# Optimization experiments

Measured on AMD Instinct MI355X. Metric: run time of the kernel, lower is better.

The kernel has to match this reference:

```python
import jax, jax.numpy as jnp
import numpy as np

HEADS = 8


def setup_inputs() -> dict:
    key = jax.random.key(0)
    ks = jax.random.split(key, 4)
    b, n, dim, inner = 8, 1024, 512, 512
    x = jax.random.normal(ks[0], (b, n, dim), jnp.float32)
    cp_mask = jax.random.randint(ks[1], (n, n), 0, 2, jnp.int32)  # binary core-periphery mask
    w_qkv = jax.random.normal(ks[2], (dim, 3 * inner), jnp.float32) * 0.02
    w_out = jax.random.normal(ks[3], (inner, dim), jnp.float32) * 0.02
    b_out = jnp.zeros((dim,), jnp.float32)
    return {"x": x, "cp_mask": cp_mask, "w_qkv": w_qkv, "w_out": w_out,
            "b_out": b_out, "patches_in_core_nodes": 16}


def reference(x, cp_mask, w_qkv, w_out, b_out, patches_in_core_nodes):
    b, n, dim = x.shape
    inner = w_qkv.shape[1] // 3
    dh = inner // HEADS
    scale = dh ** -0.5

    qkv = x @ w_qkv                                   # [b, n, 3*inner]
    q, k, v = jnp.split(qkv, 3, axis=-1)
    split_heads = lambda t: t.reshape(b, n, HEADS, dh).transpose(0, 2, 1, 3)
    q, k, v = map(split_heads, (q, k, v))             # [b, h, n, dh]

    mask = cp_mask.astype(x.dtype)                    # [n, n]
    dots_raw = jnp.einsum('bhnd,bhmd->bhnm', q, k)    # [b, h, n, n]

    # analysis pass: per-row mean |masked score|, summed over heads (detached in original)
    nnz = jnp.count_nonzero(cp_mask, axis=1).astype(x.dtype)       # [n]
    score = (jnp.abs(dots_raw * mask) * scale).sum(axis=1).sum(axis=-1) / nnz  # [b, n]
    score = jax.lax.stop_gradient(score)
    # original: list(np.argsort(score)) then list.reverse() -> batch order reversed
    idx = jnp.argsort(score, axis=-1)[::-1]           # [b, n]

    attn = jax.nn.softmax(dots_raw * scale * mask, axis=-1)
    out = jnp.einsum('bhnm,bhmd->bhnd', attn, v)      # [b, h, n, dh]
    out = out.transpose(0, 2, 1, 3).reshape(b, n, inner)

    # sequential row swap: out[j,i] <-> out[j,idx[j,i]] using the pristine clone
    out_clone = out
    bi = jnp.arange(b)
    for i in range(1, patches_in_core_nodes + 1):
        ti = idx[:, i]                                # [b]
        out = out.at[bi, i].set(out_clone[bi, ti])
        out = out.at[bi, ti].set(out_clone[:, i])
    return out @ w_out + b_out
```

## Files before the change

### kernel.cpp

```cpp
#include <hip/hip_runtime.h>
#include <hip/hip_bf16.h>

#define NN 1024
#define DH 64
#define DIM 512
#define INNER 512
#define QKV_N 1536
#define SCALE 0.125f
#define PPITCH 72

typedef short short8 __attribute__((ext_vector_type(8)));
typedef float floatx4 __attribute__((ext_vector_type(4)));

static __device__ __forceinline__ unsigned short f2bf(float x) {
  __hip_bfloat16 h = __float2bfloat16(x);
  unsigned short u;
  __builtin_memcpy(&u, &h, 2);
  return u;
}
static __device__ __forceinline__ void splitbf(float x, unsigned short& hi, unsigned short& lo) {
  __hip_bfloat16 h = __float2bfloat16(x);
  float hf = __bfloat162float(h);
  __hip_bfloat16 l = __float2bfloat16(x - hf);
  __builtin_memcpy(&hi, &h, 2);
  __builtin_memcpy(&lo, &l, 2);
}
static __device__ __forceinline__ void gll16(const unsigned short* g, unsigned short* l) {
  __builtin_amdgcn_global_load_lds(
      (const __attribute__((address_space(1))) unsigned int*)g,
      (__attribute__((address_space(3))) unsigned int*)l, 16, 0, 0);
}

__global__ __launch_bounds__(64) void nnz_kernel(const int* __restrict__ mask,
                                                 float* __restrict__ nnzf,
                                                 unsigned long long* __restrict__ Mbits) {
  int row = blockIdx.x;
  int lane = threadIdx.x;
  const int* mrow = mask + (size_t)row * NN;
  int tot = 0;
  for (int mt = 0; mt < 16; ++mt) {
    unsigned long long bits = __ballot(mrow[mt * 64 + lane] != 0);
    if (lane == 0) {
      Mbits[(size_t)mt * NN + row] = bits;
      tot += __popcll(bits);
    }
  }
  if (lane == 0) nnzf[row] = (float)tot;
}

__global__ __launch_bounds__(256) void split_kernel(const float* __restrict__ in,
                                                    unsigned short* __restrict__ hi,
                                                    unsigned short* __restrict__ lo,
                                                    int n4) {
  int i = blockIdx.x * 256 + threadIdx.x;
  if (i >= n4) return;
  float4 v = ((const float4*)in)[i];
  ushort4 h, l;
  splitbf(v.x, h.x, l.x);
  splitbf(v.y, h.y, l.y);
  splitbf(v.z, h.z, l.z);
  splitbf(v.w, h.w, l.w);
  ((ushort4*)hi)[i] = h;
  ((ushort4*)lo)[i] = l;
}

__global__ __launch_bounds__(256) void tsplit_kernel(const float* __restrict__ in, int K, int N,
                                                     unsigned short* __restrict__ hiT,
                                                     unsigned short* __restrict__ loT) {
  __shared__ float tile[32][33];
  int n0 = blockIdx.x * 32, k0 = blockIdx.y * 32;
  int t = threadIdx.x;
  int tn = t & 31, tk = t >> 5;
#pragma unroll
  for (int i = 0; i < 32; i += 8)
    tile[tk + i][tn] = in[(size_t)(k0 + tk + i) * N + n0 + tn];
  __syncthreads();
#pragma unroll
  for (int i = 0; i < 32; i += 8) {
    int n = tk + i;
    float v = tile[tn][n];
    unsigned short h, l;
    splitbf(v, h, l);
    hiT[(size_t)(n0 + n) * K + k0 + tn] = h;
    loT[(size_t)(n0 + n) * K + k0 + tn] = l;
  }
}

__global__ __launch_bounds__(256) void qkv_mfma(const unsigned short* __restrict__ xhi,
                                                const unsigned short* __restrict__ xlo,
                                                const unsigned short* __restrict__ bhiT,
                                                const unsigned short* __restrict__ bloT,
                                                unsigned short* __restrict__ qhi,
                                                unsigned short* __restrict__ qlo,
                                                unsigned short* __restrict__ khi,
                                                unsigned short* __restrict__ klo,
                                                unsigned short* __restrict__ vT) {
  __shared__ __align__(16) unsigned char smemQ[67584];
  unsigned short* planeS = (unsigned short*)smemQ;
  float* ct = (float*)smemQ;

  int l = blockIdx.x;
  int by = l & 63, bx = l >> 6;
  int r0 = by * 128, c0 = bx * 128;
  int which = c0 >> 9;
  bool split3 = (which != 2);
  int t = threadIdx.x;
  int lane = t & 63, w = t >> 6;
  int wr = w >> 1, wc = w & 1;
  int s = lane & 15, q4 = lane >> 4;
  int sx7 = s & 7;
  int r8 = lane >> 3, j7 = lane & 7;
  int colsw = ((j7 ^ r8) << 3);

  const unsigned short* gsrc;
  int tb;
  if (w == 0) { gsrc = xhi; tb = r0; }
  else if (w == 1) { gsrc = xlo; tb = r0; }
  else if (w == 2) { gsrc = bhiT; tb = c0; }
  else { gsrc = bloT; tb = c0; }
  unsigned short* lp = planeS + w * 8192;
  const unsigned short* gp = gsrc + (size_t)(tb + r8) * DIM + colsw;
  bool doStage = split3 || (w == 0) || (w == 2);

  const unsigned short* Ah = planeS;
  const unsigned short* Al = planeS + 8192;
  const unsigned short* Bh = planeS + 16384;
  const unsigned short* Bl = planeS + 24576;

  floatx4 acc[4][4];
#pragma unroll
  for (int mi = 0; mi < 4; ++mi)
#pragma unroll
    for (int ni = 0; ni < 4; ++ni) { acc[mi][ni][0] = 0.f; acc[mi][ni][1] = 0.f; acc[mi][ni][2] = 0.f; acc[mi][ni][3] = 0.f; }

  for (int kt = 0; kt < DIM; kt += 64) {
    __syncthreads();
    if (doStage) {
#pragma unroll
      for (int ii = 0; ii < 16; ++ii)
        gll16(gp + (size_t)ii * 8 * DIM + kt, lp + ii * 512);
    }
    __syncthreads();
#pragma unroll
    for (int ks2 = 0; ks2 < 2; ++ks2) {
      int pc = ((ks2 * 4 + q4) ^ sx7) << 3;
      short8 ah[4], al[4], bhf[4], blf[4];
#pragma unroll
      for (int mi = 0; mi < 4; ++mi) {
        int ra = (wr * 64 + mi * 16 + s) * 64 + pc;
        ah[mi] = *(const short8*)&Ah[ra];
        if (split3) al[mi] = *(const short8*)&Al[ra];
      }
#pragma unroll
      for (int ni = 0; ni < 4; ++ni) {
        int rb = (wc * 64 + ni * 16 + s) * 64 + pc;
        bhf[ni] = *(const short8*)&Bh[rb];
        if (split3) blf[ni] = *(const short8*)&Bl[rb];
      }
#pragma unroll
      for (int mi = 0; mi < 4; ++mi)
#pragma unroll
        for (int ni = 0; ni < 4; ++ni) {
          if (split3) {
            acc[mi][ni] = __builtin_amdgcn_mfma_f32_16x16x32_bf16(al[mi], bhf[ni], acc[mi][ni], 0, 0, 0);
            acc[mi][ni] = __builtin_amdgcn_mfma_f32_16x16x32_bf16(ah[mi], blf[ni], acc[mi][ni], 0, 0, 0);
          }
          acc[mi][ni] = __builtin_amdgcn_mfma_f32_16x16x32_bf16(ah[mi], bhf[ni], acc[mi][ni], 0, 0, 0);
        }
    }
  }

  __syncthreads();
  if (which != 2) {
    float sc = (which == 0) ? SCALE : 1.0f;
#pragma unroll
    for (int mi = 0; mi < 4; ++mi)
#pragma unroll
      for (int ni = 0; ni < 4; ++ni)
#pragma unroll
        for (int i = 0; i < 4; ++i)
          ct[(wr * 64 + mi * 16 + q4 * 4 + i) * 132 + (wc * 64 + ni * 16 + s)] = acc[mi][ni][i] * sc;
  } else {
#pragma unroll
    for (int mi = 0; mi < 4; ++mi)
#pragma unroll
      for (int ni = 0; ni < 4; ++ni)
#pragma unroll
        for (int i = 0; i < 4; ++i)
          ct[(wc * 64 + ni * 16 + s) * 132 + (wr * 64 + mi * 16 + q4 * 4 + i)] = acc[mi][ni][i];
  }
  __syncthreads();
  if (which != 2) {
    int tr = t >> 1, ch = t & 1;
    int R = r0 + tr, b = R >> 10, n = R & 1023;
    int h0 = ((c0 & 511) >> 6) + ch;
    unsigned short* dhi = (which == 0) ? qhi : khi;
    unsigned short* dlo = (which == 0) ? qlo : klo;
    size_t go = ((size_t)(((b << 3) + h0) << 10) + n) * DH;
#pragma unroll
    for (int u = 0; u < 4; ++u) {
      const float* src = &ct[tr * 132 + ch * 64 + u * 16];
      short8 h8a, h8b, l8a, l8b;
#pragma unroll
      for (int e = 0; e < 8; ++e) {
        unsigned short hh, ll;
        splitbf(src[e], hh, ll);
        h8a[e] = (short)hh; l8a[e] = (short)ll;
        splitbf(src[8 + e], hh, ll);
        h8b[e] = (short)hh; l8b[e] = (short)ll;
      }
      *(short8*)&dhi[go + u * 16] = h8a;
      *(short8*)&dhi[go + u * 16 + 8] = h8b;
      *(short8*)&dlo[go + u * 16] = l8a;
      *(short8*)&dlo[go + u * 16 + 8] = l8b;
    }
  } else {
    int cr = t >> 1, th = t & 1;
    int b = r0 >> 10;
    int hglob = ((c0 & 511) >> 6) + (cr >> 6);
    int d = cr & 63;
    int n0 = (r0 & 1023) + th * 64;
    size_t go = ((size_t)(((b << 3) + hglob) * DH) + d) * NN + n0;
#pragma unroll
    for (int u = 0; u < 4; ++u) {
      const float* src = &ct[cr * 132 + th * 64 + u * 16];
      short8 o0, o1;
#pragma unroll
      for (int e = 0; e < 8; ++e) {
        o0[e] = (short)f2bf(src[e]);
        o1[e] = (short)f2bf(src[8 + e]);
      }
      *(short8*)&vT[go + u * 16] = o0;
      *(short8*)&vT[go + u * 16 + 8] = o1;
    }
  }
}

__global__ __launch_bounds__(256, 4) void attn_kernel(const unsigned short* __restrict__ qhi,
                                                      const unsigned short* __restrict__ qlo,
                                                      const unsigned short* __restrict__ khi,
                                                      const unsigned short* __restrict__ klo,
                                                      const unsigned short* __restrict__ vT,
                                                      const unsigned long long* __restrict__ MbT,
                                                      unsigned short* __restrict__ ohi,
                                                      unsigned short* __restrict__ olo,
                                                      float* __restrict__ sph) {
  int l = blockIdx.y * 16 + blockIdx.x;
  int k = l >> 3;
  int rb = k & 15;
  int bh = (l & 7) + 8 * (k >> 4);
  int b = bh >> 3, h = bh & 7;
  int row0 = rb * 64;
  int t = threadIdx.x;
  int lane = t & 63, w = t >> 6;
  int q4 = lane >> 4, s = lane & 15;
  int sx7 = s & 7;
  int gr = 16 * w + s;
  int r8 = lane >> 3, j7 = lane & 7;
  int colsw = ((j7 ^ r8) << 3);

  __shared__ __align__(16) unsigned short stageS[3 * 4096];
  __shared__ __align__(16) unsigned short Ps[64 * PPITCH];
  __shared__ unsigned long long Mb[64];
  unsigned short* Khs = stageS;
  unsigned short* Kls = stageS + 4096;
  unsigned short* Vts = stageS + 8192;
  float* Ofl = (float*)stageS;

  const unsigned short* khp = khi + ((size_t)bh * NN + 16 * w + r8) * DH + colsw;
  const unsigned short* klp = klo + ((size_t)bh * NN + 16 * w + r8) * DH + colsw;
  const unsigned short* vtp = vT + ((size_t)bh * DH + 16 * w + r8) * NN + colsw;

  short8 aqh[2], aql[2];
  {
    size_t qb0 = ((size_t)bh * NN + row0 + gr) * DH;
#pragma unroll
    for (int ks = 0; ks < 2; ++ks) {
      aqh[ks] = *(const short8*)&qhi[qb0 + ks * 32 + q4 * 8];
      aql[ks] = *(const short8*)&qlo[qb0 + ks * 32 + q4 * 8];
    }
  }

  floatx4 Oacc[4];
  float Lacc[4], Sco[4];
#pragma unroll
  for (int j = 0; j < 4; ++j) { Oacc[j][0] = 0.f; Oacc[j][1] = 0.f; Oacc[j][2] = 0.f; Oacc[j][3] = 0.f; }
#pragma unroll
  for (int i = 0; i < 4; ++i) { Lacc[i] = 0.f; Sco[i] = 0.f; }

  for (int mt = 0; mt < 16; ++mt) {
    __syncthreads();
#pragma unroll
    for (int ii = 0; ii < 2; ++ii) {
      int lofs = (16 * w + 8 * ii) * 64;
      gll16(khp + (size_t)mt * 64 * DH + (size_t)ii * 8 * DH, Khs + lofs);
      gll16(klp + (size_t)mt * 64 * DH + (size_t)ii * 8 * DH, Kls + lofs);
      gll16(vtp + (size_t)mt * 64 + (size_t)ii * 8 * NN, Vts + lofs);
    }
    if (t < 64) Mb[t] = MbT[(size_t)mt * NN + row0 + t];
    __syncthreads();

    floatx4 Sf[4];
#pragma unroll
    for (int j = 0; j < 4; ++j) { Sf[j][0] = 0.f; Sf[j][1] = 0.f; Sf[j][2] = 0.f; Sf[j][3] = 0.f; }
#pragma unroll
    for (int ks = 0; ks < 2; ++ks) {
      int pc = ((ks * 4 + q4) ^ sx7) << 3;
#pragma unroll
      for (int j = 0; j < 4; ++j) {
        int rk = (16 * j + s) * 64 + pc;
        short8 kh8 = *(const short8*)&Khs[rk];
        short8 kl8 = *(const short8*)&Kls[rk];
        Sf[j] = __builtin_amdgcn_mfma_f32_16x16x32_bf16(aql[ks], kh8, Sf[j], 0, 0, 0);
        Sf[j] = __builtin_amdgcn_mfma_f32_16x16x32_bf16(aqh[ks], kl8, Sf[j], 0, 0, 0);
        Sf[j] = __builtin_amdgcn_mfma_f32_16x16x32_bf16(aqh[ks], kh8, Sf[j], 0, 0, 0);
      }
    }

    unsigned long long mb[4];
#pragma unroll
    for (int i = 0; i < 4; ++i) mb[i] = Mb[16 * w + 4 * q4 + i];
    unsigned short pw[4][4];
#pragma unroll
    for (int j = 0; j < 4; ++j) {
#pragma unroll
      for (int i = 0; i < 4; ++i) {
        float sv = Sf[j][i];
        float mf = ((mb[i] >> (16 * j + s)) & 1ULL) ? 1.0f : 0.0f;
        Sco[i] += fabsf(sv) * mf;
        float p = __expf(sv * mf);
        Lacc[i] += p;
        pw[i][j] = f2bf(p);
      }
    }

#pragma unroll
    for (int i = 0; i < 4; ++i)
#pragma unroll
      for (int j = 0; j < 4; ++j) Ps[(16 * w + 4 * q4 + i) * PPITCH + 16 * j + s] = pw[i][j];

#pragma unroll
    for (int ks = 0; ks < 2; ++ks) {
      int mm0 = ks * 32 + q4 * 8;
      short8 ap = *(const short8*)&Ps[gr * PPITCH + mm0];
      int pc = ((ks * 4 + q4) ^ sx7) << 3;
#pragma unroll
      for (int j = 0; j < 4; ++j) {
        short8 bv = *(const short8*)&Vts[(16 * j + s) * 64 + pc];
        Oacc[j] = __builtin_amdgcn_mfma_f32_16x16x32_bf16(ap, bv, Oacc[j], 0, 0, 0);
      }
    }
  }

#pragma unroll
  for (int off = 1; off < 16; off <<= 1) {
#pragma unroll
    for (int i = 0; i < 4; ++i) {
      Lacc[i] += __shfl_xor(Lacc[i], off, 16);
      Sco[i] += __shfl_xor(Sco[i], off, 16);
    }
  }
  if (s == 0) {
#pragma unroll
    for (int i = 0; i < 4; ++i)
      sph[((size_t)bh << 10) + row0 + 16 * w + 4 * q4 + i] = Sco[i];
  }

  __syncthreads();
#pragma unroll
  for (int i = 0; i < 4; ++i) {
    float iv = 1.0f / Lacc[i];
#pragma unroll
    for (int j = 0; j < 4; ++j)
      Ofl[(16 * w + 4 * q4 + i) * 68 + 16 * j + s] = Oacc[j][i] * iv;
  }
  __syncthreads();
  {
    int tr = t >> 2, dq = t & 3;
    int r = row0 + tr;
    size_t go = ((size_t)((b << 10) + r)) * INNER + (h << 6) + dq * 16;
    const float* src = &Ofl[tr * 68 + dq * 16];
    short8 h8a, h8b, l8a, l8b;
#pragma unroll
    for (int e = 0; e < 8; ++e) {
      unsigned short hh, ll;
      splitbf(src[e], hh, ll);
      h8a[e] = (short)hh; l8a[e] = (short)ll;
      splitbf(src[8 + e], hh, ll);
      h8b[e] = (short)hh; l8b[e] = (short)ll;
    }
    *(short8*)&ohi[go] = h8a;
    *(short8*)&ohi[go + 8] = h8b;
    *(short8*)&olo[go] = l8a;
    *(short8*)&olo[go + 8] = l8b;
  }
}

__global__ __launch_bounds__(256) void score_select(const float* __restrict__ sph,
                                                    const float* __restrict__ nnzf,
                                                    const int* __restrict__ pic_ptr,
                                                    int* __restrict__ asc) {
  int bb = blockIdx.x;
  int t = threadIdx.x;
  int cnt = pic_ptr[0] + 1;
  float v[4];
#pragma unroll
  for (int i = 0; i < 4; ++i) {
    int r = t + 256 * i;
    float sv = 0.f;
#pragma unroll
    for (int h = 0; h < 8; ++h) sv += sph[(size_t)(((bb << 3) + h) << 10) + r];
    v[i] = sv / nnzf[r];
  }
  __shared__ float wv[4];
  __shared__ int wi[4];
  __shared__ int bsel;
  for (int sel = 0; sel < cnt; ++sel) {
    float bv = v[0];
    int bi = t;
#pragma unroll
    for (int i = 1; i < 4; ++i) {
      if (v[i] < bv) { bv = v[i]; bi = t + 256 * i; }
    }
#pragma unroll
    for (int off = 1; off < 64; off <<= 1) {
      float ov = __shfl_xor(bv, off, 64);
      int oi = __shfl_xor(bi, off, 64);
      if (ov < bv || (ov == bv && oi < bi)) { bv = ov; bi = oi; }
    }
    if ((t & 63) == 0) { wv[t >> 6] = bv; wi[t >> 6] = bi; }
    __syncthreads();
    if (t == 0) {
      float B = wv[0]; int I = wi[0];
#pragma unroll
      for (int q = 1; q < 4; ++q) {
        if (wv[q] < B || (wv[q] == B && wi[q] < I)) { B = wv[q]; I = wi[q]; }
      }
      bsel = I;
      asc[bb * 32 + sel] = I;
    }
    __syncthreads();
    int wloc = bsel - t;
    if (wloc >= 0 && (wloc & 255) == 0 && wloc < 1024) v[wloc >> 8] = 3.4e38f;
    __syncthreads();
  }
}

__global__ __launch_bounds__(256) void build_src(const int* __restrict__ asc,
                                                 const int* __restrict__ pic_ptr,
                                                 int* __restrict__ src) {
  int bi = blockIdx.x;
  int t = threadIdx.x;
  for (int r = t; r < 1024; r += 256) src[bi * 1024 + r] = r;
  __syncthreads();
  if (t == 0) {
    int pic = pic_ptr[0];
    const int* a = &asc[(7 - bi) * 32];
    for (int i = 1; i <= pic; ++i) {
      int ti = a[i];
      src[bi * 1024 + i] = ti;
      src[bi * 1024 + ti] = i;
    }
  }
}

__global__ __launch_bounds__(256) void out_mfma(const unsigned short* __restrict__ ahi,
                                                const unsigned short* __restrict__ alo,
                                                const unsigned short* __restrict__ bhiT,
                                                const unsigned short* __restrict__ bloT,
                                                const float* __restrict__ bias,
                                                const int* __restrict__ src,
                                                float* __restrict__ C) {
  __shared__ __align__(16) unsigned short planeS[4 * 8192];
  int l = blockIdx.x;
  int by = l & 63, bx = l >> 6;
  int r0 = by * 128, c0 = bx * 128;
  int t = threadIdx.x;
  int lane = t & 63, w = t >> 6;
  int wr = w >> 1, wc = w & 1;
  int s = lane & 15, q4 = lane >> 4;
  int sx7 = s & 7;
  int r8 = lane >> 3, j7 = lane & 7;
  int colsw = ((j7 ^ r8) << 3);
  int bb1024 = (r0 >> 10) << 10;

  int srcrow[16];
  if (w < 2) {
#pragma unroll
    for (int ii = 0; ii < 16; ++ii) srcrow[ii] = src[r0 + ii * 8 + r8];
  }
  const unsigned short* gsrc = (w == 0) ? ahi : (w == 1) ? alo : (w == 2) ? bhiT : bloT;
  unsigned short* lp = planeS + w * 8192;

  const unsigned short* Ah = planeS;
  const unsigned short* Al = planeS + 8192;
  const unsigned short* Bh = planeS + 16384;
  const unsigned short* Bl = planeS + 24576;

  floatx4 acc[4][4];
#pragma unroll
  for (int mi = 0; mi < 4; ++mi)
#pragma unroll
    for (int ni = 0; ni < 4; ++ni) { acc[mi][ni][0] = 0.f; acc[mi][ni][1] = 0.f; acc[mi][ni][2] = 0.f; acc[mi][ni][3] = 0.f; }

  for (int kt = 0; kt < INNER; kt += 64) {
    __syncthreads();
    if (w < 2) {
#pragma unroll
      for (int ii = 0; ii < 16; ++ii)
        gll16(gsrc + (size_t)(bb1024 + srcrow[ii]) * INNER + kt + colsw, lp + ii * 512);
    } else {
#pragma unroll
      for (int ii = 0; ii < 16; ++ii)
        gll16(gsrc + (size_t)(c0 + ii * 8 + r8) * INNER + kt + colsw, lp + ii * 512);
    }
    __syncthreads();
#pragma unroll
    for (int ks2 = 0; ks2 < 2; ++ks2) {
      int pc = ((ks2 * 4 + q4) ^ sx7) << 3;
      short8 ah[4], al[4], bhf[4], blf[4];
#pragma unroll
      for (int mi = 0; mi < 4; ++mi) {
        int ra = (wr * 64 + mi * 16 + s) * 64 + pc;
        ah[mi] = *(const short8*)&Ah[ra];
        al[mi] = *(const short8*)&Al[ra];
      }
#pragma unroll
      for (int ni = 0; ni < 4; ++ni) {
        int rb = (wc * 64 + ni * 16 + s) * 64 + pc;
        bhf[ni] = *(const short8*)&Bh[rb];
        blf[ni] = *(const short8*)&Bl[rb];
      }
#pragma unroll
      for (int mi = 0; mi < 4; ++mi)
#pragma unroll
        for (int ni = 0; ni < 4; ++ni) {
          acc[mi][ni] = __builtin_amdgcn_mfma_f32_16x16x32_bf16(al[mi], bhf[ni], acc[mi][ni], 0, 0, 0);
          acc[mi][ni] = __builtin_amdgcn_mfma_f32_16x16x32_bf16(ah[mi], blf[ni], acc[mi][ni], 0, 0, 0);
          acc[mi][ni] = __builtin_amdgcn_mfma_f32_16x16x32_bf16(ah[mi], bhf[ni], acc[mi][ni], 0, 0, 0);
        }
    }
  }

#pragma unroll
  for (int ni = 0; ni < 4; ++ni) {
    int Cl = c0 + wc * 64 + ni * 16 + s;
    float bv = bias[Cl];
#pragma unroll
    for (int mi = 0; mi < 4; ++mi)
#pragma unroll
      for (int i = 0; i < 4; ++i) {
        int R = r0 + wr * 64 + mi * 16 + q4 * 4 + i;
        C[(size_t)R * DIM + Cl] = acc[mi][ni][i] + bv;
      }
  }
}

extern "C" void kernel_launch(void* const* d_in, const int* in_sizes, int n_in,
                              void* d_out, int out_size, void* d_ws, size_t ws_size,
                              hipStream_t stream) {
  const float* x      = (const float*)d_in[0];
  const int*   cpmask = (const int*)d_in[1];
  const float* w_qkv  = (const float*)d_in[2];
  const float* w_out  = (const float*)d_in[3];
  const float* b_out  = (const float*)d_in[4];
  const int*   pic    = (const int*)d_in[5];
  float* out = (float*)d_out;

  unsigned short* xhi   = (unsigned short*)d_ws;
  unsigned short* xlo   = xhi + 4194304;
  unsigned short* wqhiT = xlo + 4194304;
  unsigned short* wqloT = wqhiT + 786432;
  unsigned short* wohiT = wqloT + 786432;
  unsigned short* woloT = wohiT + 262144;
  unsigned short* qhi   = woloT + 262144;
  unsigned short* qlo   = qhi + 4194304;
  unsigned short* khi   = qlo + 4194304;
  unsigned short* klo   = khi + 4194304;
  unsigned short* vbp   = klo + 4194304;
  float* sph  = (float*)(vbp + 4194304);
  float* sc   = sph + 65536;
  float* nnzf = sc + 8192;
  int*   asc  = (int*)(nnzf + 1024);
  int*   src  = asc + 512;
  unsigned long long* Mbits = (unsigned long long*)(src + 8192);
  unsigned short* vTp = (unsigned short*)(Mbits + 16384);

  unsigned short* ohi = xhi;
  unsigned short* olo = xlo;

  hipLaunchKernelGGL(nnz_kernel,    dim3(1024),    dim3(64),  0, stream, cpmask, nnzf, Mbits);
  hipLaunchKernelGGL(split_kernel,  dim3(4096),    dim3(256), 0, stream, x, xhi, xlo, 1048576);
  hipLaunchKernelGGL(tsplit_kernel, dim3(48, 16),  dim3(256), 0, stream, w_qkv, DIM, QKV_N, wqhiT, wqloT);
  hipLaunchKernelGGL(tsplit_kernel, dim3(16, 16),  dim3(256), 0, stream, w_out, INNER, DIM, wohiT, woloT);
  hipLaunchKernelGGL(qkv_mfma,      dim3(768),     dim3(256), 0, stream, xhi, xlo, wqhiT, wqloT,
                     qhi, qlo, khi, klo, vTp);
  hipLaunchKernelGGL(attn_kernel,   dim3(16, 64),  dim3(256), 0, stream, qhi, qlo, khi, klo, vTp,
                     Mbits, ohi, olo, sph);
  hipLaunchKernelGGL(score_select,  dim3(8),       dim3(256), 0, stream, sph, nnzf, pic, asc);
  hipLaunchKernelGGL(build_src,     dim3(8),       dim3(256), 0, stream, asc, pic, src);
  hipLaunchKernelGGL(out_mfma,      dim3(256),     dim3(256), 0, stream, ohi, olo, wohiT, woloT,
                     b_out, src, out);
}
```

Baseline: 226.5 us.

## Replace LDS staging with direct global loads in QKV, attention and output GEMMs

Removes the global_load_lds staging into shared memory and its barriers from the QKV projection, attention and output projection kernels, so each wave reads MFMA operands straight from global memory and relies on the caches for reuse. The QKV epilogue now stages half the tile at a time through a smaller shared buffer. The output GEMM tile narrows to 128x64 and the grid doubles. The attention kernel drops its occupancy hint. This cuts LDS use and synchronisation, but adds redundant uncoalesced global loads and cache pressure, especially for the repeated K/V reads in attention.

```diff
diff --git a/kernel.cpp b/kernel.cpp
--- a/kernel.cpp
+++ b/kernel.cpp
@@ -24,11 +24,6 @@
   __hip_bfloat16 l = __float2bfloat16(x - hf);
   __builtin_memcpy(&hi, &h, 2);
   __builtin_memcpy(&lo, &l, 2);
-}
-static __device__ __forceinline__ void gll16(const unsigned short* g, unsigned short* l) {
-  __builtin_amdgcn_global_load_lds(
-      (const __attribute__((address_space(1))) unsigned int*)g,
-      (__attribute__((address_space(3))) unsigned int*)l, 16, 0, 0);
 }
 
 __global__ __launch_bounds__(64) void nnz_kernel(const int* __restrict__ mask,
@@ -95,9 +90,7 @@
                                                 unsigned short* __restrict__ khi,
                                                 unsigned short* __restrict__ klo,
                                                 unsigned short* __restrict__ vT) {
-  __shared__ __align__(16) unsigned char smemQ[67584];
-  unsigned short* planeS = (unsigned short*)smemQ;
-  float* ct = (float*)smemQ;
+  __shared__ __align__(16) float ct[64 * 132];
 
   int l = blockIdx.x;
   int by = l & 63, bx = l >> 6;
@@ -108,24 +101,11 @@
   int lane = t & 63, w = t >> 6;
   int wr = w >> 1, wc = w & 1;
   int s = lane & 15, q4 = lane >> 4;
-  int sx7 = s & 7;
-  int r8 = lane >> 3, j7 = lane & 7;
-  int colsw = ((j7 ^ r8) << 3);
-
-  const unsigned short* gsrc;
-  int tb;
-  if (w == 0) { gsrc = xhi; tb = r0; }
-  else if (w == 1) { gsrc = xlo; tb = r0; }
-  else if (w == 2) { gsrc = bhiT; tb = c0; }
-  else { gsrc = bloT; tb = c0; }
-  unsigned short* lp = planeS + w * 8192;
-  const unsigned short* gp = gsrc + (size_t)(tb + r8) * DIM + colsw;
-  bool doStage = split3 || (w == 0) || (w == 2);
-
-  const unsigned short* Ah = planeS;
-  const unsigned short* Al = planeS + 8192;
-  const unsigned short* Bh = planeS + 16384;
-  const unsigned short* Bl = planeS + 24576;
+
+  const unsigned short* aH = xhi + (size_t)(r0 + wr * 64 + s) * DIM + q4 * 8;
+  const unsigned short* aL = xlo + (size_t)(r0 + wr * 64 + s) * DIM + q4 * 8;
+  const unsigned short* bH = bhiT + (size_t)(c0 + wc * 64 + s) * DIM + q4 * 8;
+  const unsigned short* bL = bloT + (size_t)(c0 + wc * 64 + s) * DIM + q4 * 8;
 
   floatx4 acc[4][4];
 #pragma unroll
@@ -133,118 +113,116 @@
 #pragma unroll
     for (int ni = 0; ni < 4; ++ni) { acc[mi][ni][0] = 0.f; acc[mi][ni][1] = 0.f; acc[mi][ni][2] = 0.f; acc[mi][ni][3] = 0.f; }
 
-  for (int kt = 0; kt < DIM; kt += 64) {
-    __syncthreads();
-    if (doStage) {
-#pragma unroll
-      for (int ii = 0; ii < 16; ++ii)
-        gll16(gp + (size_t)ii * 8 * DIM + kt, lp + ii * 512);
-    }
-    __syncthreads();
-#pragma unroll
-    for (int ks2 = 0; ks2 < 2; ++ks2) {
-      int pc = ((ks2 * 4 + q4) ^ sx7) << 3;
-      short8 ah[4], al[4], bhf[4], blf[4];
-#pragma unroll
-      for (int mi = 0; mi < 4; ++mi) {
-        int ra = (wr * 64 + mi * 16 + s) * 64 + pc;
-        ah[mi] = *(const short8*)&Ah[ra];
-        if (split3) al[mi] = *(const short8*)&Al[ra];
-      }
+#pragma unroll
+  for (int ks = 0; ks < 16; ++ks) {
+    int ko = ks * 32;
+    short8 ah[4], al[4], bh8[4], bl8[4];
+#pragma unroll
+    for (int mi = 0; mi < 4; ++mi) {
+      ah[mi] = *(const short8*)(aH + (size_t)mi * 16 * DIM + ko);
+      if (split3) al[mi] = *(const short8*)(aL + (size_t)mi * 16 * DIM + ko);
+    }
+#pragma unroll
+    for (int ni = 0; ni < 4; ++ni) {
+      bh8[ni] = *(const short8*)(bH + (size_t)ni * 16 * DIM + ko);
+      if (split3) bl8[ni] = *(const short8*)(bL + (size_t)ni * 16 * DIM + ko);
+    }
+#pragma unroll
+    for (int mi = 0; mi < 4; ++mi)
 #pragma unroll
       for (int ni = 0; ni < 4; ++ni) {
-        int rb = (wc * 64 + ni * 16 + s) * 64 + pc;
-        bhf[ni] = *(const short8*)&Bh[rb];
-        if (split3) blf[ni] = *(const short8*)&Bl[rb];
-      }
-#pragma unroll
-      for (int mi = 0; mi < 4; ++mi)
-#pragma unroll
-        for (int ni = 0; ni < 4; ++ni) {
-          if (split3) {
-            acc[mi][ni] = __builtin_amdgcn_mfma_f32_16x16x32_bf16(al[mi], bhf[ni], acc[mi][ni], 0, 0, 0);
-            acc[mi][ni] = __builtin_amdgcn_mfma_f32_16x16x32_bf16(ah[mi], blf[ni], acc[mi][ni], 0, 0, 0);
-          }
-          acc[mi][ni] = __builtin_amdgcn_mfma_f32_16x16x32_bf16(ah[mi], bhf[ni], acc[mi][ni], 0, 0, 0);
+        if (split3) {
+          acc[mi][ni] = __builtin_amdgcn_mfma_f32_16x16x32_bf16(al[mi], bh8[ni], acc[mi][ni], 0, 0, 0);
+          acc[mi][ni] = __builtin_amdgcn_mfma_f32_16x16x32_bf16(ah[mi], bl8[ni], acc[mi][ni], 0, 0, 0);
         }
-    }
-  }
-
-  __syncthreads();
+        acc[mi][ni] = __builtin_amdgcn_mfma_f32_16x16x32_bf16(ah[mi], bh8[ni], acc[mi][ni], 0, 0, 0);
+      }
+  }
+
+  int b = r0 >> 10;
   if (which != 2) {
-    float sc = (which == 0) ? SCALE : 1.0f;
-#pragma unroll
-    for (int mi = 0; mi < 4; ++mi)
-#pragma unroll
-      for (int ni = 0; ni < 4; ++ni)
-#pragma unroll
-        for (int i = 0; i < 4; ++i)
-          ct[(wr * 64 + mi * 16 + q4 * 4 + i) * 132 + (wc * 64 + ni * 16 + s)] = acc[mi][ni][i] * sc;
-  } else {
-#pragma unroll
-    for (int mi = 0; mi < 4; ++mi)
-#pragma unroll
-      for (int ni = 0; ni < 4; ++ni)
-#pragma unroll
-        for (int i = 0; i < 4; ++i)
-          ct[(wc * 64 + ni * 16 + s) * 132 + (wr * 64 + mi * 16 + q4 * 4 + i)] = acc[mi][ni][i];
-  }
-  __syncthreads();
-  if (which != 2) {
-    int tr = t >> 1, ch = t & 1;
-    int R = r0 + tr, b = R >> 10, n = R & 1023;
-    int h0 = ((c0 & 511) >> 6) + ch;
+    float scf = (which == 0) ? SCALE : 1.0f;
     unsigned short* dhi = (which == 0) ? qhi : khi;
     unsigned short* dlo = (which == 0) ? qlo : klo;
-    size_t go = ((size_t)(((b << 3) + h0) << 10) + n) * DH;
-#pragma unroll
-    for (int u = 0; u < 4; ++u) {
-      const float* src = &ct[tr * 132 + ch * 64 + u * 16];
-      short8 h8a, h8b, l8a, l8b;
-#pragma unroll
-      for (int e = 0; e < 8; ++e) {
-        unsigned short hh, ll;
-        splitbf(src[e], hh, ll);
-        h8a[e] = (short)hh; l8a[e] = (short)ll;
-        splitbf(src[8 + e], hh, ll);
-        h8b[e] = (short)hh; l8b[e] = (short)ll;
-      }
-      *(short8*)&dhi[go + u * 16] = h8a;
-      *(short8*)&dhi[go + u * 16 + 8] = h8b;
-      *(short8*)&dlo[go + u * 16] = l8a;
-      *(short8*)&dlo[go + u * 16 + 8] = l8b;
+    int hb = (c0 & 511) >> 6;
+#pragma unroll
+    for (int p = 0; p < 2; ++p) {
+      if (p) __syncthreads();
+      if (wr == p) {
+#pragma unroll
+        for (int mi = 0; mi < 4; ++mi)
+#pragma unroll
+          for (int ni = 0; ni < 4; ++ni)
+#pragma unroll
+            for (int i = 0; i < 4; ++i)
+              ct[(mi * 16 + q4 * 4 + i) * 132 + (wc * 64 + ni * 16 + s)] = acc[mi][ni][i] * scf;
+      }
+      __syncthreads();
+      {
+        int tr = t >> 2, seg = t & 3;
+        int h = hb + (seg >> 1);
+        int d0 = (seg & 1) * 32;
+        int n = (r0 & 1023) + 64 * p + tr;
+        size_t go = ((size_t)(((b << 3) + h) << 10) + n) * DH + d0;
+        const float* src = &ct[tr * 132 + seg * 32];
+        short8 h8[4], l8[4];
+#pragma unroll
+        for (int u = 0; u < 4; ++u)
+#pragma unroll
+          for (int e = 0; e < 8; ++e) {
+            unsigned short hh, ll;
+            splitbf(src[u * 8 + e], hh, ll);
+            h8[u][e] = (short)hh; l8[u][e] = (short)ll;
+          }
+#pragma unroll
+        for (int u = 0; u < 4; ++u) {
+          *(short8*)&dhi[go + u * 8] = h8[u];
+          *(short8*)&dlo[go + u * 8] = l8[u];
+        }
+      }
     }
   } else {
-    int cr = t >> 1, th = t & 1;
-    int b = r0 >> 10;
-    int hglob = ((c0 & 511) >> 6) + (cr >> 6);
-    int d = cr & 63;
-    int n0 = (r0 & 1023) + th * 64;
-    size_t go = ((size_t)(((b << 3) + hglob) * DH) + d) * NN + n0;
-#pragma unroll
-    for (int u = 0; u < 4; ++u) {
-      const float* src = &ct[cr * 132 + th * 64 + u * 16];
-      short8 o0, o1;
-#pragma unroll
-      for (int e = 0; e < 8; ++e) {
-        o0[e] = (short)f2bf(src[e]);
-        o1[e] = (short)f2bf(src[8 + e]);
-      }
-      *(short8*)&vT[go + u * 16] = o0;
-      *(short8*)&vT[go + u * 16 + 8] = o1;
-    }
-  }
-}
-
-__global__ __launch_bounds__(256, 4) void attn_kernel(const unsigned short* __restrict__ qhi,
-                                                      const unsigned short* __restrict__ qlo,
-                                                      const unsigned short* __restrict__ khi,
-                                                      const unsigned short* __restrict__ klo,
-                                                      const unsigned short* __restrict__ vT,
-                                                      const unsigned long long* __restrict__ MbT,
-                                                      unsigned short* __restrict__ ohi,
-                                                      unsigned short* __restrict__ olo,
-                                                      float* __restrict__ sph) {
+    int hb = (c0 & 511) >> 6;
+#pragma unroll
+    for (int p = 0; p < 2; ++p) {
+      if (p) __syncthreads();
+      if (wc == p) {
+#pragma unroll
+        for (int mi = 0; mi < 4; ++mi)
+#pragma unroll
+          for (int ni = 0; ni < 4; ++ni)
+#pragma unroll
+            for (int i = 0; i < 4; ++i)
+              ct[(ni * 16 + s) * 132 + (wr * 64 + mi * 16 + q4 * 4 + i)] = acc[mi][ni][i];
+      }
+      __syncthreads();
+      {
+        int d = t >> 2, nseg = t & 3;
+        int h = hb + p;
+        int n0 = (r0 & 1023) + nseg * 32;
+        size_t go = ((size_t)(((b << 3) + h) * DH) + d) * NN + n0;
+        const float* src = &ct[d * 132 + nseg * 32];
+        short8 o[4];
+#pragma unroll
+        for (int u = 0; u < 4; ++u)
+#pragma unroll
+          for (int e = 0; e < 8; ++e) o[u][e] = (short)f2bf(src[u * 8 + e]);
+#pragma unroll
+        for (int u = 0; u < 4; ++u) *(short8*)&vT[go + u * 8] = o[u];
+      }
+    }
+  }
+}
+
+__global__ __launch_bounds__(256) void attn_kernel(const unsigned short* __restrict__ qhi,
+                                                   const unsigned short* __restrict__ qlo,
+                                                   const unsigned short* __restrict__ khi,
+                                                   const unsigned short* __restrict__ klo,
+                                                   const unsigned short* __restrict__ vT,
+                                                   const unsigned long long* __restrict__ MbT,
+                                                   unsigned short* __restrict__ ohi,
+                                                   unsigned short* __restrict__ olo,
+                                                   float* __restrict__ sph) {
   int l = blockIdx.y * 16 + blockIdx.x;
   int k = l >> 3;
   int rb = k & 15;
@@ -254,22 +232,11 @@
   int t = threadIdx.x;
   int lane = t & 63, w = t >> 6;
   int q4 = lane >> 4, s = lane & 15;
-  int sx7 = s & 7;
   int gr = 16 * w + s;
-  int r8 = lane >> 3, j7 = lane & 7;
-  int colsw = ((j7 ^ r8) << 3);
-
-  __shared__ __align__(16) unsigned short stageS[3 * 4096];
-  __shared__ __align__(16) unsigned short Ps[64 * PPITCH];
-  __shared__ unsigned long long Mb[64];
-  unsigned short* Khs = stageS;
-  unsigned short* Kls = stageS + 4096;
-  unsigned short* Vts = stageS + 8192;
-  float* Ofl = (float*)stageS;
-
-  const unsigned short* khp = khi + ((size_t)bh * NN + 16 * w + r8) * DH + colsw;
-  const unsigned short* klp = klo + ((size_t)bh * NN + 16 * w + r8) * DH + colsw;
-  const unsigned short* vtp = vT + ((size_t)bh * DH + 16 * w + r8) * NN + colsw;
+
+  __shared__ __align__(16) unsigned char smemA[64 * 68 * 4];
+  unsigned short* Ps = (unsigned short*)smemA;
+  float* Ofl = (float*)smemA;
 
   short8 aqh[2], aql[2];
   {
@@ -288,29 +255,23 @@
 #pragma unroll
   for (int i = 0; i < 4; ++i) { Lacc[i] = 0.f; Sco[i] = 0.f; }
 
+  const unsigned short* kHb = khi + (size_t)bh * NN * DH + q4 * 8;
+  const unsigned short* kLb = klo + (size_t)bh * NN * DH + q4 * 8;
+  const unsigned short* vTb = vT + (size_t)bh * DH * NN + q4 * 8;
+
   for (int mt = 0; mt < 16; ++mt) {
-    __syncthreads();
-#pragma unroll
-    for (int ii = 0; ii < 2; ++ii) {
-      int lofs = (16 * w + 8 * ii) * 64;
-      gll16(khp + (size_t)mt * 64 * DH + (size_t)ii * 8 * DH, Khs + lofs);
-      gll16(klp + (size_t)mt * 64 * DH + (size_t)ii * 8 * DH, Kls + lofs);
-      gll16(vtp + (size_t)mt * 64 + (size_t)ii * 8 * NN, Vts + lofs);
-    }
-    if (t < 64) Mb[t] = MbT[(size_t)mt * NN + row0 + t];
-    __syncthreads();
+    int m0 = mt * 64;
 
     floatx4 Sf[4];
 #pragma unroll
     for (int j = 0; j < 4; ++j) { Sf[j][0] = 0.f; Sf[j][1] = 0.f; Sf[j][2] = 0.f; Sf[j][3] = 0.f; }
 #pragma unroll
     for (int ks = 0; ks < 2; ++ks) {
-      int pc = ((ks * 4 + q4) ^ sx7) << 3;
 #pragma unroll
       for (int j = 0; j < 4; ++j) {
-        int rk = (16 * j + s) * 64 + pc;
-        short8 kh8 = *(const short8*)&Khs[rk];
-        short8 kl8 = *(const short8*)&Kls[rk];
+        size_t go = (size_t)(m0 + 16 * j + s) * DH + ks * 32;
+        short8 kh8 = *(const short8*)(kHb + go);
+        short8 kl8 = *(const short8*)(kLb + go);
         Sf[j] = __builtin_amdgcn_mfma_f32_16x16x32_bf16(aql[ks], kh8, Sf[j], 0, 0, 0);
         Sf[j] = __builtin_amdgcn_mfma_f32_16x16x32_bf16(aqh[ks], kl8, Sf[j], 0, 0, 0);
         Sf[j] = __builtin_amdgcn_mfma_f32_16x16x32_bf16(aqh[ks], kh8, Sf[j], 0, 0, 0);
@@ -318,8 +279,12 @@
     }
 
     unsigned long long mb[4];
-#pragma unroll
-    for (int i = 0; i < 4; ++i) mb[i] = Mb[16 * w + 4 * q4 + i];
+    {
+      const unsigned long long* mp = &MbT[(size_t)mt * NN + row0 + 16 * w + 4 * q4];
+#pragma unroll
+      for (int i = 0; i < 4; ++i) mb[i] = mp[i];
+    }
+
     unsigned short pw[4][4];
 #pragma unroll
     for (int j = 0; j < 4; ++j) {
@@ -341,12 +306,10 @@
 
 #pragma unroll
     for (int ks = 0; ks < 2; ++ks) {
-      int mm0 = ks * 32 + q4 * 8;
-      short8 ap = *(const short8*)&Ps[gr * PPITCH + mm0];
-      int pc = ((ks * 4 + q4) ^ sx7) << 3;
+      short8 ap = *(const short8*)&Ps[gr * PPITCH + ks * 32 + q4 * 8];
 #pragma unroll
       for (int j = 0; j < 4; ++j) {
-        short8 bv = *(const short8*)&Vts[(16 * j + s) * 64 + pc];
+        short8 bv = *(const short8*)(vTb + (size_t)(16 * j + s) * NN + m0 + ks * 32);
         Oacc[j] = __builtin_amdgcn_mfma_f32_16x16x32_bf16(ap, bv, Oacc[j], 0, 0, 0);
       }
     }
@@ -471,80 +434,56 @@
                                                 const float* __restrict__ bias,
                                                 const int* __restrict__ src,
                                                 float* __restrict__ C) {
-  __shared__ __align__(16) unsigned short planeS[4 * 8192];
   int l = blockIdx.x;
   int by = l & 63, bx = l >> 6;
-  int r0 = by * 128, c0 = bx * 128;
+  int r0 = by * 128, c0 = bx * 64;
   int t = threadIdx.x;
   int lane = t & 63, w = t >> 6;
   int wr = w >> 1, wc = w & 1;
   int s = lane & 15, q4 = lane >> 4;
-  int sx7 = s & 7;
-  int r8 = lane >> 3, j7 = lane & 7;
-  int colsw = ((j7 ^ r8) << 3);
   int bb1024 = (r0 >> 10) << 10;
 
-  int srcrow[16];
-  if (w < 2) {
-#pragma unroll
-    for (int ii = 0; ii < 16; ++ii) srcrow[ii] = src[r0 + ii * 8 + r8];
-  }
-  const unsigned short* gsrc = (w == 0) ? ahi : (w == 1) ? alo : (w == 2) ? bhiT : bloT;
-  unsigned short* lp = planeS + w * 8192;
-
-  const unsigned short* Ah = planeS;
-  const unsigned short* Al = planeS + 8192;
-  const unsigned short* Bh = planeS + 16384;
-  const unsigned short* Bl = planeS + 24576;
-
-  floatx4 acc[4][4];
+  int grow[4];
 #pragma unroll
   for (int mi = 0; mi < 4; ++mi)
-#pragma unroll
-    for (int ni = 0; ni < 4; ++ni) { acc[mi][ni][0] = 0.f; acc[mi][ni][1] = 0.f; acc[mi][ni][2] = 0.f; acc[mi][ni][3] = 0.f; }
-
-  for (int kt = 0; kt < INNER; kt += 64) {
-    __syncthreads();
-    if (w < 2) {
-#pragma unroll
-      for (int ii = 0; ii < 16; ++ii)
-        gll16(gsrc + (size_t)(bb1024 + srcrow[ii]) * INNER + kt + colsw, lp + ii * 512);
-    } else {
-#pragma unroll
-      for (int ii = 0; ii < 16; ++ii)
-        gll16(gsrc + (size_t)(c0 + ii * 8 + r8) * INNER + kt + colsw, lp + ii * 512);
-    }
-    __syncthreads();
-#pragma unroll
-    for (int ks2 = 0; ks2 < 2; ++ks2) {
-      int pc = ((ks2 * 4 + q4) ^ sx7) << 3;
-      short8 ah[4], al[4], bhf[4], blf[4];
-#pragma unroll
-      for (int mi = 0; mi < 4; ++mi) {
-        int ra = (wr * 64 + mi * 16 + s) * 64 + pc;
-        ah[mi] = *(const short8*)&Ah[ra];
-        al[mi] = *(const short8*)&Al[ra];
-      }
-#pragma unroll
-      for (int ni = 0; ni < 4; ++ni) {
-        int rb = (wc * 64 + ni * 16 + s) * 64 + pc;
-        bhf[ni] = *(const short8*)&Bh[rb];
-        blf[ni] = *(const short8*)&Bl[rb];
-      }
-#pragma unroll
-      for (int mi = 0; mi < 4; ++mi)
-#pragma unroll
-        for (int ni = 0; ni < 4; ++ni) {
-          acc[mi][ni] = __builtin_amdgcn_mfma_f32_16x16x32_bf16(al[mi], bhf[ni], acc[mi][ni], 0, 0, 0);
-          acc[mi][ni] = __builtin_amdgcn_mfma_f32_16x16x32_bf16(ah[mi], blf[ni], acc[mi][ni], 0, 0, 0);
-          acc[mi][ni] = __builtin_amdgcn_mfma_f32_16x16x32_bf16(ah[mi], bhf[ni], acc[mi][ni], 0, 0, 0);
-        }
-    }
-  }
-
-#pragma unroll
-  for (int ni = 0; ni < 4; ++ni) {
-    int Cl = c0 + wc * 64 + ni * 16 + s;
+    grow[mi] = bb1024 + src[r0 + wr * 64 + mi * 16 + s];
+
+  const unsigned short* bH = bhiT + (size_t)(c0 + wc * 32 + s) * INNER + q4 * 8;
+  const unsigned short* bL = bloT + (size_t)(c0 + wc * 32 + s) * INNER + q4 * 8;
+
+  floatx4 acc[4][2];
+#pragma unroll
+  for (int mi = 0; mi < 4; ++mi)
+#pragma unroll
+    for (int ni = 0; ni < 2; ++ni) { acc[mi][ni][0] = 0.f; acc[mi][ni][1] = 0.f; acc[mi][ni][2] = 0.f; acc[mi][ni][3] = 0.f; }
+
+#pragma unroll
+  for (int ks = 0; ks < 16; ++ks) {
+    int ko = ks * 32 + q4 * 8;
+    short8 ah[4], al[4], bh8[2], bl8[2];
+#pragma unroll
+    for (int mi = 0; mi < 4; ++mi) {
+      ah[mi] = *(const short8*)(ahi + (size_t)grow[mi] * INNER + ko);
+      al[mi] = *(const short8*)(alo + (size_t)grow[mi] * INNER + ko);
+    }
+#pragma unroll
+    for (int ni = 0; ni < 2; ++ni) {
+      bh8[ni] = *(const short8*)(bH + (size_t)ni * 16 * INNER + ks * 32);
+      bl8[ni] = *(const short8*)(bL + (size_t)ni * 16 * INNER + ks * 32);
+    }
+#pragma unroll
+    for (int mi = 0; mi < 4; ++mi)
+#pragma unroll
+      for (int ni = 0; ni < 2; ++ni) {
+        acc[mi][ni] = __builtin_amdgcn_mfma_f32_16x16x32_bf16(al[mi], bh8[ni], acc[mi][ni], 0, 0, 0);
+        acc[mi][ni] = __builtin_amdgcn_mfma_f32_16x16x32_bf16(ah[mi], bl8[ni], acc[mi][ni], 0, 0, 0);
+        acc[mi][ni] = __builtin_amdgcn_mfma_f32_16x16x32_bf16(ah[mi], bh8[ni], acc[mi][ni], 0, 0, 0);
+      }
+  }
+
+#pragma unroll
+  for (int ni = 0; ni < 2; ++ni) {
+    int Cl = c0 + wc * 32 + ni * 16 + s;
     float bv = bias[Cl];
 #pragma unroll
     for (int mi = 0; mi < 4; ++mi)
@@ -599,6 +538,6 @@
                      Mbits, ohi, olo, sph);
   hipLaunchKernelGGL(score_select,  dim3(8),       dim3(256), 0, stream, sph, nnzf, pic, asc);
   hipLaunchKernelGGL(build_src,     dim3(8),       dim3(256), 0, stream, asc, pic, src);
-  hipLaunchKernelGGL(out_mfma,      dim3(256),     dim3(256), 0, stream, ohi, olo, wohiT, woloT,
+  hipLaunchKernelGGL(out_mfma,      dim3(512),     dim3(256), 0, stream, ohi, olo, wohiT, woloT,
                      b_out, src, out);
 }
```

Result: slower. 429.7 us (+89.7%).

## Double attention query tile per block and make score selection single-wave

Applied to the files above, without the earlier changes.

The attention kernel now gives each block 128 query rows instead of 64, with each wave handling two 16-row subtiles. Every K/V tile staged in shared memory is therefore reused across twice as many queries, halving global K/V traffic and the number of stage barriers. The cost is more registers, fewer blocks (512), and a lower occupancy hint. Separately, score_select runs as a single 64-lane wave with 16 values per lane, removing the shared-memory reduction and the block barriers from each top-k iteration.

```diff
diff --git a/kernel.cpp b/kernel.cpp
--- a/kernel.cpp
+++ b/kernel.cpp
@@ -236,7 +236,7 @@
   }
 }
 
-__global__ __launch_bounds__(256, 4) void attn_kernel(const unsigned short* __restrict__ qhi,
+__global__ __launch_bounds__(256, 3) void attn_kernel(const unsigned short* __restrict__ qhi,
                                                       const unsigned short* __restrict__ qlo,
                                                       const unsigned short* __restrict__ khi,
                                                       const unsigned short* __restrict__ klo,
@@ -245,48 +245,49 @@
                                                       unsigned short* __restrict__ ohi,
                                                       unsigned short* __restrict__ olo,
                                                       float* __restrict__ sph) {
-  int l = blockIdx.y * 16 + blockIdx.x;
-  int k = l >> 3;
-  int rb = k & 15;
-  int bh = (l & 7) + 8 * (k >> 4);
+  int l = blockIdx.x;
+  int bh = l & 63, rb = l >> 6;
   int b = bh >> 3, h = bh & 7;
-  int row0 = rb * 64;
+  int row0 = rb * 128;
   int t = threadIdx.x;
   int lane = t & 63, w = t >> 6;
   int q4 = lane >> 4, s = lane & 15;
   int sx7 = s & 7;
-  int gr = 16 * w + s;
   int r8 = lane >> 3, j7 = lane & 7;
   int colsw = ((j7 ^ r8) << 3);
 
-  __shared__ __align__(16) unsigned short stageS[3 * 4096];
-  __shared__ __align__(16) unsigned short Ps[64 * PPITCH];
-  __shared__ unsigned long long Mb[64];
-  unsigned short* Khs = stageS;
-  unsigned short* Kls = stageS + 4096;
-  unsigned short* Vts = stageS + 8192;
-  float* Ofl = (float*)stageS;
+  __shared__ __align__(16) unsigned char smemA[43008];
+  unsigned short* Khs = (unsigned short*)smemA;
+  unsigned short* Kls = Khs + 4096;
+  unsigned short* Vts = Khs + 8192;
+  unsigned short* Ps  = Khs + 12288;
+  float* Ofl = (float*)smemA;
+  __shared__ unsigned long long Mb[128];
 
   const unsigned short* khp = khi + ((size_t)bh * NN + 16 * w + r8) * DH + colsw;
   const unsigned short* klp = klo + ((size_t)bh * NN + 16 * w + r8) * DH + colsw;
   const unsigned short* vtp = vT + ((size_t)bh * DH + 16 * w + r8) * NN + colsw;
 
-  short8 aqh[2], aql[2];
-  {
-    size_t qb0 = ((size_t)bh * NN + row0 + gr) * DH;
+  short8 aqh[2][2], aql[2][2];
+#pragma unroll
+  for (int st = 0; st < 2; ++st) {
+    size_t qb0 = ((size_t)bh * NN + row0 + 32 * w + 16 * st + s) * DH;
 #pragma unroll
     for (int ks = 0; ks < 2; ++ks) {
-      aqh[ks] = *(const short8*)&qhi[qb0 + ks * 32 + q4 * 8];
-      aql[ks] = *(const short8*)&qlo[qb0 + ks * 32 + q4 * 8];
-    }
-  }
-
-  floatx4 Oacc[4];
-  float Lacc[4], Sco[4];
-#pragma unroll
-  for (int j = 0; j < 4; ++j) { Oacc[j][0] = 0.f; Oacc[j][1] = 0.f; Oacc[j][2] = 0.f; Oacc[j][3] = 0.f; }
-#pragma unroll
-  for (int i = 0; i < 4; ++i) { Lacc[i] = 0.f; Sco[i] = 0.f; }
+      aqh[st][ks] = *(const short8*)&qhi[qb0 + ks * 32 + q4 * 8];
+      aql[st][ks] = *(const short8*)&qlo[qb0 + ks * 32 + q4 * 8];
+    }
+  }
+
+  floatx4 Oacc[2][4];
+  float Lacc[2][4], Sco[2][4];
+#pragma unroll
+  for (int st = 0; st < 2; ++st) {
+#pragma unroll
+    for (int j = 0; j < 4; ++j) { Oacc[st][j][0] = 0.f; Oacc[st][j][1] = 0.f; Oacc[st][j][2] = 0.f; Oacc[st][j][3] = 0.f; }
+#pragma unroll
+    for (int i = 0; i < 4; ++i) { Lacc[st][i] = 0.f; Sco[st][i] = 0.f; }
+  }
 
   for (int mt = 0; mt < 16; ++mt) {
     __syncthreads();
@@ -297,130 +298,135 @@
       gll16(klp + (size_t)mt * 64 * DH + (size_t)ii * 8 * DH, Kls + lofs);
       gll16(vtp + (size_t)mt * 64 + (size_t)ii * 8 * NN, Vts + lofs);
     }
-    if (t < 64) Mb[t] = MbT[(size_t)mt * NN + row0 + t];
+    if (t < 128) Mb[t] = MbT[(size_t)mt * NN + row0 + t];
     __syncthreads();
 
-    floatx4 Sf[4];
-#pragma unroll
-    for (int j = 0; j < 4; ++j) { Sf[j][0] = 0.f; Sf[j][1] = 0.f; Sf[j][2] = 0.f; Sf[j][3] = 0.f; }
-#pragma unroll
-    for (int ks = 0; ks < 2; ++ks) {
-      int pc = ((ks * 4 + q4) ^ sx7) << 3;
+#pragma unroll
+    for (int st = 0; st < 2; ++st) {
+      floatx4 Sf[4];
+#pragma unroll
+      for (int j = 0; j < 4; ++j) { Sf[j][0] = 0.f; Sf[j][1] = 0.f; Sf[j][2] = 0.f; Sf[j][3] = 0.f; }
+#pragma unroll
+      for (int ks = 0; ks < 2; ++ks) {
+        int pc = ((ks * 4 + q4) ^ sx7) << 3;
+#pragma unroll
+        for (int j = 0; j < 4; ++j) {
+          int rk = (16 * j + s) * 64 + pc;
+          short8 kh8 = *(const short8*)&Khs[rk];
+          short8 kl8 = *(const short8*)&Kls[rk];
+          Sf[j] = __builtin_amdgcn_mfma_f32_16x16x32_bf16(aql[st][ks], kh8, Sf[j], 0, 0, 0);
+          Sf[j] = __builtin_amdgcn_mfma_f32_16x16x32_bf16(aqh[st][ks], kl8, Sf[j], 0, 0, 0);
+          Sf[j] = __builtin_amdgcn_mfma_f32_16x16x32_bf16(aqh[st][ks], kh8, Sf[j], 0, 0, 0);
+        }
+      }
+
+      unsigned long long mb[4];
+#pragma unroll
+      for (int i = 0; i < 4; ++i) mb[i] = Mb[32 * w + 16 * st + 4 * q4 + i];
+      unsigned short pw[4][4];
 #pragma unroll
       for (int j = 0; j < 4; ++j) {
-        int rk = (16 * j + s) * 64 + pc;
-        short8 kh8 = *(const short8*)&Khs[rk];
-        short8 kl8 = *(const short8*)&Kls[rk];
-        Sf[j] = __builtin_amdgcn_mfma_f32_16x16x32_bf16(aql[ks], kh8, Sf[j], 0, 0, 0);
-        Sf[j] = __builtin_amdgcn_mfma_f32_16x16x32_bf16(aqh[ks], kl8, Sf[j], 0, 0, 0);
-        Sf[j] = __builtin_amdgcn_mfma_f32_16x16x32_bf16(aqh[ks], kh8, Sf[j], 0, 0, 0);
-      }
-    }
-
-    unsigned long long mb[4];
-#pragma unroll
-    for (int i = 0; i < 4; ++i) mb[i] = Mb[16 * w + 4 * q4 + i];
-    unsigned short pw[4][4];
-#pragma unroll
-    for (int j = 0; j < 4; ++j) {
+#pragma unroll
+        for (int i = 0; i < 4; ++i) {
+          float sv = Sf[j][i];
+          float mf = ((mb[i] >> (16 * j + s)) & 1ULL) ? 1.0f : 0.0f;
+          Sco[st][i] += fabsf(sv) * mf;
+          float p = __expf(sv * mf);
+          Lacc[st][i] += p;
+          pw[i][j] = f2bf(p);
+        }
+      }
+
+#pragma unroll
+      for (int i = 0; i < 4; ++i)
+#pragma unroll
+        for (int j = 0; j < 4; ++j)
+          Ps[(32 * w + 16 * st + 4 * q4 + i) * PPITCH + 16 * j + s] = pw[i][j];
+
+#pragma unroll
+      for (int ks = 0; ks < 2; ++ks) {
+        short8 ap = *(const short8*)&Ps[(32 * w + 16 * st + s) * PPITCH + ks * 32 + q4 * 8];
+        int pc = ((ks * 4 + q4) ^ sx7) << 3;
+#pragma unroll
+        for (int j = 0; j < 4; ++j) {
+          short8 bv = *(const short8*)&Vts[(16 * j + s) * 64 + pc];
+          Oacc[st][j] = __builtin_amdgcn_mfma_f32_16x16x32_bf16(ap, bv, Oacc[st][j], 0, 0, 0);
+        }
+      }
+    }
+  }
+
+#pragma unroll
+  for (int st = 0; st < 2; ++st) {
+#pragma unroll
+    for (int off = 1; off < 16; off <<= 1) {
 #pragma unroll
       for (int i = 0; i < 4; ++i) {
-        float sv = Sf[j][i];
-        float mf = ((mb[i] >> (16 * j + s)) & 1ULL) ? 1.0f : 0.0f;
-        Sco[i] += fabsf(sv) * mf;
-        float p = __expf(sv * mf);
-        Lacc[i] += p;
-        pw[i][j] = f2bf(p);
-      }
-    }
-
-#pragma unroll
-    for (int i = 0; i < 4; ++i)
-#pragma unroll
-      for (int j = 0; j < 4; ++j) Ps[(16 * w + 4 * q4 + i) * PPITCH + 16 * j + s] = pw[i][j];
-
-#pragma unroll
-    for (int ks = 0; ks < 2; ++ks) {
-      int mm0 = ks * 32 + q4 * 8;
-      short8 ap = *(const short8*)&Ps[gr * PPITCH + mm0];
-      int pc = ((ks * 4 + q4) ^ sx7) << 3;
-#pragma unroll
-      for (int j = 0; j < 4; ++j) {
-        short8 bv = *(const short8*)&Vts[(16 * j + s) * 64 + pc];
-        Oacc[j] = __builtin_amdgcn_mfma_f32_16x16x32_bf16(ap, bv, Oacc[j], 0, 0, 0);
-      }
-    }
-  }
-
-#pragma unroll
-  for (int off = 1; off < 16; off <<= 1) {
+        Lacc[st][i] += __shfl_xor(Lacc[st][i], off, 16);
+        Sco[st][i] += __shfl_xor(Sco[st][i], off, 16);
+      }
+    }
+    if (s == 0) {
+#pragma unroll
+      for (int i = 0; i < 4; ++i)
+        sph[((size_t)bh << 10) + row0 + 32 * w + 16 * st + 4 * q4 + i] = Sco[st][i];
+    }
+  }
+
+  __syncthreads();
+#pragma unroll
+  for (int st = 0; st < 2; ++st)
 #pragma unroll
     for (int i = 0; i < 4; ++i) {
-      Lacc[i] += __shfl_xor(Lacc[i], off, 16);
-      Sco[i] += __shfl_xor(Sco[i], off, 16);
-    }
-  }
-  if (s == 0) {
-#pragma unroll
-    for (int i = 0; i < 4; ++i)
-      sph[((size_t)bh << 10) + row0 + 16 * w + 4 * q4 + i] = Sco[i];
-  }
-
-  __syncthreads();
-#pragma unroll
-  for (int i = 0; i < 4; ++i) {
-    float iv = 1.0f / Lacc[i];
-#pragma unroll
-    for (int j = 0; j < 4; ++j)
-      Ofl[(16 * w + 4 * q4 + i) * 68 + 16 * j + s] = Oacc[j][i] * iv;
-  }
+      float iv = 1.0f / Lacc[st][i];
+#pragma unroll
+      for (int j = 0; j < 4; ++j)
+        Ofl[(32 * w + 16 * st + 4 * q4 + i) * 68 + 16 * j + s] = Oacc[st][j][i] * iv;
+    }
   __syncthreads();
   {
-    int tr = t >> 2, dq = t & 3;
+    int tr = t >> 1, half = t & 1;
     int r = row0 + tr;
-    size_t go = ((size_t)((b << 10) + r)) * INNER + (h << 6) + dq * 16;
-    const float* src = &Ofl[tr * 68 + dq * 16];
-    short8 h8a, h8b, l8a, l8b;
-#pragma unroll
-    for (int e = 0; e < 8; ++e) {
-      unsigned short hh, ll;
-      splitbf(src[e], hh, ll);
-      h8a[e] = (short)hh; l8a[e] = (short)ll;
-      splitbf(src[8 + e], hh, ll);
-      h8b[e] = (short)hh; l8b[e] = (short)ll;
-    }
-    *(short8*)&ohi[go] = h8a;
-    *(short8*)&ohi[go + 8] = h8b;
-    *(short8*)&olo[go] = l8a;
-    *(short8*)&olo[go + 8] = l8b;
-  }
-}
-
-__global__ __launch_bounds__(256) void score_select(const float* __restrict__ sph,
-                                                    const float* __restrict__ nnzf,
-                                                    const int* __restrict__ pic_ptr,
-                                                    int* __restrict__ asc) {
+    size_t go = ((size_t)((b << 10) + r)) * INNER + (h << 6) + half * 32;
+    const float* src = &Ofl[tr * 68 + half * 32];
+#pragma unroll
+    for (int u = 0; u < 4; ++u) {
+      short8 h8, l8;
+#pragma unroll
+      for (int e = 0; e < 8; ++e) {
+        unsigned short hh, ll;
+        splitbf(src[u * 8 + e], hh, ll);
+        h8[e] = (short)hh; l8[e] = (short)ll;
+      }
+      *(short8*)&ohi[go + u * 8] = h8;
+      *(short8*)&olo[go + u * 8] = l8;
+    }
+  }
+}
+
+__global__ __launch_bounds__(64) void score_select(const float* __restrict__ sph,
+                                                   const float* __restrict__ nnzf,
+                                                   const int* __restrict__ pic_ptr,
+                                                   int* __restrict__ asc) {
   int bb = blockIdx.x;
-  int t = threadIdx.x;
+  int lane = threadIdx.x;
   int cnt = pic_ptr[0] + 1;
-  float v[4];
-#pragma unroll
-  for (int i = 0; i < 4; ++i) {
-    int r = t + 256 * i;
+  float v[16];
+#pragma unroll
+  for (int i = 0; i < 16; ++i) {
+    int r = i * 64 + lane;
     float sv = 0.f;
 #pragma unroll
     for (int h = 0; h < 8; ++h) sv += sph[(size_t)(((bb << 3) + h) << 10) + r];
     v[i] = sv / nnzf[r];
   }
-  __shared__ float wv[4];
-  __shared__ int wi[4];
-  __shared__ int bsel;
   for (int sel = 0; sel < cnt; ++sel) {
     float bv = v[0];
-    int bi = t;
-#pragma unroll
-    for (int i = 1; i < 4; ++i) {
-      if (v[i] < bv) { bv = v[i]; bi = t + 256 * i; }
+    int bi = lane;
+#pragma unroll
+    for (int i = 1; i < 16; ++i) {
+      int r = i * 64 + lane;
+      if (v[i] < bv) { bv = v[i]; bi = r; }
     }
 #pragma unroll
     for (int off = 1; off < 64; off <<= 1) {
@@ -428,21 +434,14 @@
       int oi = __shfl_xor(bi, off, 64);
       if (ov < bv || (ov == bv && oi < bi)) { bv = ov; bi = oi; }
     }
-    if ((t & 63) == 0) { wv[t >> 6] = bv; wi[t >> 6] = bi; }
-    __syncthreads();
-    if (t == 0) {
-      float B = wv[0]; int I = wi[0];
-#pragma unroll
-      for (int q = 1; q < 4; ++q) {
-        if (wv[q] < B || (wv[q] == B && wi[q] < I)) { B = wv[q]; I = wi[q]; }
-      }
-      bsel = I;
-      asc[bb * 32 + sel] = I;
-    }
-    __syncthreads();
-    int wloc = bsel - t;
-    if (wloc >= 0 && (wloc & 255) == 0 && wloc < 1024) v[wloc >> 8] = 3.4e38f;
-    __syncthreads();
+    if (lane == 0) asc[bb * 32 + sel] = bi;
+    int selidx = __shfl(bi, 0, 64);
+    if ((selidx & 63) == lane) {
+      int slot = selidx >> 6;
+#pragma unroll
+      for (int i = 0; i < 16; ++i)
+        if (i == slot) v[i] = 3.4e38f;
+    }
   }
 }
 
@@ -595,9 +594,9 @@
   hipLaunchKernelGGL(tsplit_kernel, dim3(16, 16),  dim3(256), 0, stream, w_out, INNER, DIM, wohiT, woloT);
   hipLaunchKernelGGL(qkv_mfma,      dim3(768),     dim3(256), 0, stream, xhi, xlo, wqhiT, wqloT,
                      qhi, qlo, khi, klo, vTp);
-  hipLaunchKernelGGL(attn_kernel,   dim3(16, 64),  dim3(256), 0, stream, qhi, qlo, khi, klo, vTp,
+  hipLaunchKernelGGL(attn_kernel,   dim3(512),     dim3(256), 0, stream, qhi, qlo, khi, klo, vTp,
                      Mbits, ohi, olo, sph);
-  hipLaunchKernelGGL(score_select,  dim3(8),       dim3(256), 0, stream, sph, nnzf, pic, asc);
+  hipLaunchKernelGGL(score_select,  dim3(8),       dim3(64),  0, stream, sph, nnzf, pic, asc);
   hipLaunchKernelGGL(build_src,     dim3(8),       dim3(256), 0, stream, asc, pic, src);
   hipLaunchKernelGGL(out_mfma,      dim3(256),     dim3(256), 0, stream, ohi, olo, wohiT, woloT,
                      b_out, src, out);
```

Result: slower. 231.5 us (+2.2%).
